# Performance work log

Hardware: AMD Instinct MI355X
Metric: run time of the kernel (lower is better)

Reference implementation:

```python
import jax, jax.numpy as jnp
import numpy as np

EMBED_DIM = 1024
NUM_HEADS = 16
DIM_K = EMBED_DIM // NUM_HEADS
B, S = 2, 2048


def setup_inputs() -> dict:
    key = jax.random.key(0)
    ks = jax.random.split(key, 7)
    scale = 1.0 / np.sqrt(EMBED_DIM)
    return {
        "query": jax.random.normal(ks[0], (B, S, EMBED_DIM), dtype=jnp.float32),
        "key": jax.random.normal(ks[1], (B, S, EMBED_DIM), dtype=jnp.float32),
        "value": jax.random.normal(ks[2], (B, S, EMBED_DIM), dtype=jnp.float32),
        "Wq": jax.random.normal(ks[3], (EMBED_DIM, EMBED_DIM), dtype=jnp.float32) * scale,
        "Wk": jax.random.normal(ks[4], (EMBED_DIM, EMBED_DIM), dtype=jnp.float32) * scale,
        "Wv": jax.random.normal(ks[5], (EMBED_DIM, EMBED_DIM), dtype=jnp.float32) * scale,
        "Wo": jax.random.normal(ks[6], (EMBED_DIM, EMBED_DIM), dtype=jnp.float32) * scale,
    }


def reference(query, key, value, Wq, Wk, Wv, Wo):
    b, s, e = query.shape
    # nn.Linear: y = x @ W.T  (bias=False)
    def proj(x, W):
        y = x @ W.T  # [b, s, e]
        return y.reshape(b, -1, NUM_HEADS, DIM_K).transpose(0, 2, 1, 3)  # [b, h, s, dk]

    q = proj(query, Wq)
    k = proj(key, Wk)
    v = proj(value, Wv)

    # attention: scores = q k^T / sqrt(dk); softmax; @ v  (dropout p=0 in eval)
    scores = jnp.einsum("bhqd,bhkd->bhqk", q, k) / jnp.sqrt(jnp.float32(DIM_K))
    attn = jax.nn.softmax(scores, axis=-1)
    x = jnp.einsum("bhqk,bhkd->bhqd", attn, v)  # [b, h, s, dk]

    x = x.transpose(0, 2, 1, 3).reshape(b, -1, e)  # merge heads
    return x @ Wo.T
```

## Files before the change

### kernel.cpp

```cpp
#include <hip/hip_runtime.h>
#include <hip/hip_bf16.h>
#include <stdint.h>

#define EMBED 1024
#define NHEAD 16
#define DKD   64
#define BATCH 2
#define SEQ   2048
#define MROWS (BATCH*SEQ)

typedef __attribute__((ext_vector_type(8)))  short bf16x8;
typedef __attribute__((ext_vector_type(4)))  float f32x4;
typedef __attribute__((ext_vector_type(16))) float f32x16;
typedef unsigned short u16;
typedef unsigned int   u32;
typedef __attribute__((ext_vector_type(4))) u32 u32x4;

__device__ inline u16 f2bf(float f) {
  return __builtin_bit_cast(u16, __float2bfloat16(f));
}

__device__ inline u32 cvtpk(float lo, float hi) {
  u32 r;
  asm("v_cvt_pk_bf16_f32 %0, %1, %2" : "=v"(r) : "v"(lo), "v"(hi));
  return r;
}

__device__ inline void plswap(u32& x, u32& y) {
  asm volatile("v_permlane32_swap_b32 %0, %1" : "+v"(x), "+v"(y));
}

__device__ inline void gload_lds16(const u16* g, u16* l) {
  __builtin_amdgcn_global_load_lds(
      (const __attribute__((address_space(1))) u32*)(const void*)g,
      (__attribute__((address_space(3))) u32*)(void*)l, 16, 0, 0);
}

__global__ __launch_bounds__(256) void cast_all(
    const float* __restrict__ s0, const float* __restrict__ s1,
    const float* __restrict__ s2, const float* __restrict__ s3,
    const float* __restrict__ s4, const float* __restrict__ s5,
    const float* __restrict__ s6,
    u16* __restrict__ d0, u16* __restrict__ d1, u16* __restrict__ d2,
    u16* __restrict__ d3, u16* __restrict__ d4, u16* __restrict__ d5,
    u16* __restrict__ d6) {
  const int y = blockIdx.y;
  const float* s; u16* d; int n4;
  switch (y) {
    case 0: s = s0; d = d0; n4 = MROWS*EMBED/4; break;
    case 1: s = s1; d = d1; n4 = MROWS*EMBED/4; break;
    case 2: s = s2; d = d2; n4 = MROWS*EMBED/4; break;
    case 3: s = s3; d = d3; n4 = EMBED*EMBED/4; break;
    case 4: s = s4; d = d4; n4 = EMBED*EMBED/4; break;
    case 5: s = s5; d = d5; n4 = EMBED*EMBED/4; break;
    default: s = s6; d = d6; n4 = EMBED*EMBED/4; break;
  }
  int i = blockIdx.x * 256 + threadIdx.x;
  int stride = gridDim.x * 256;
  for (int idx = i; idx < n4; idx += stride) {
    float4 f = ((const float4*)s)[idx];
    ushort4 o;
    o.x = f2bf(f.x); o.y = f2bf(f.y); o.z = f2bf(f.z); o.w = f2bf(f.w);
    ((ushort4*)d)[idx] = o;
  }
}

__global__ __launch_bounds__(256)
void gemm_qkv(const u16* __restrict__ A0, const u16* __restrict__ A1,
              const u16* __restrict__ A2, const u16* __restrict__ B0,
              const u16* __restrict__ B1, const u16* __restrict__ B2,
              u16* __restrict__ C0, u16* __restrict__ C1, u16* __restrict__ C2) {
  constexpr int K = EMBED;
  __shared__ u16 As[128 * 32];
  __shared__ u16 Bs[128 * 32];
  const int z = blockIdx.z;
  const u16* A = (z == 0) ? A0 : (z == 1) ? A1 : A2;
  const u16* B = (z == 0) ? B0 : (z == 1) ? B1 : B2;
  u16* C       = (z == 0) ? C0 : (z == 1) ? C1 : C2;

  const int t = threadIdx.x;
  const int w = t >> 6, l = t & 63;
  const int lr = l & 15, lg = l >> 4;
  const int m0 = blockIdx.x * 128;
  const int n0 = blockIdx.y * 128;
  const int wr = (w >> 1) * 64, wc = (w & 1) * 64;

  f32x4 acc[4][4] = {};

  const int srow = t >> 2;
  const int scol = (t & 3) * 8;
  const u16* Ag = A + (size_t)(m0 + srow) * K + scol;
  const u16* Bg = B + (size_t)(n0 + srow) * K + scol;
  u16* AsW = As + w * 512;
  u16* BsW = Bs + w * 512;
  const size_t rowstep = (size_t)64 * K;

  for (int k0 = 0; k0 < K; k0 += 32) {
    gload_lds16(Ag + k0,           AsW);
    gload_lds16(Ag + k0 + rowstep, AsW + 64 * 32);
    gload_lds16(Bg + k0,           BsW);
    gload_lds16(Bg + k0 + rowstep, BsW + 64 * 32);
    __syncthreads();
    bf16x8 a[4], b[4];
#pragma unroll
    for (int r = 0; r < 4; r++)
      a[r] = *(const bf16x8*)(As + (wr + r * 16 + lr) * 32 + 8 * lg);
#pragma unroll
    for (int c = 0; c < 4; c++)
      b[c] = *(const bf16x8*)(Bs + (wc + c * 16 + lr) * 32 + 8 * lg);
#pragma unroll
    for (int r = 0; r < 4; r++)
#pragma unroll
      for (int c = 0; c < 4; c++)
        acc[r][c] = __builtin_amdgcn_mfma_f32_16x16x32_bf16(a[r], b[c], acc[r][c], 0, 0, 0);
    __syncthreads();
  }

#pragma unroll
  for (int r = 0; r < 4; r++)
#pragma unroll
    for (int c = 0; c < 4; c++)
#pragma unroll
      for (int j = 0; j < 4; j++) {
        int m = m0 + wr + r * 16 + lg * 4 + j;
        int n = n0 + wc + c * 16 + lr;
        int b_ = m >> 11, s_ = m & 2047;
        int h_ = n >> 6,  d_ = n & 63;
        u16 vv = f2bf(acc[r][c][j]);
        if (z == 2)
          C[((size_t)(b_ * NHEAD + h_) * DKD + d_) * SEQ + s_] = vv;
        else
          C[(((size_t)(b_ * NHEAD + h_) * SEQ + s_) << 6) + d_] = vv;
      }
}

__global__ __launch_bounds__(256)
void gemm_out(const u16* __restrict__ A, const u16* __restrict__ B,
              float* __restrict__ C) {
  constexpr int K = EMBED, N = EMBED;
  __shared__ u16 As[64 * 32];
  __shared__ u16 Bs[128 * 32];
  const int t = threadIdx.x;
  const int w = t >> 6, l = t & 63;
  const int lr = l & 15, lg = l >> 4;
  const int m0 = blockIdx.x * 64;
  const int n0 = blockIdx.y * 128;
  const int wr = (w >> 1) * 32, wc = (w & 1) * 64;

  f32x4 acc[2][4] = {};

  const int srow = t >> 2;
  const int scol = (t & 3) * 8;
  const u16* Ag = A + (size_t)(m0 + srow) * K + scol;
  const u16* Bg = B + (size_t)(n0 + srow) * K + scol;
  u16* AsW = As + w * 512;
  u16* BsW = Bs + w * 512;
  const size_t rowstep = (size_t)64 * K;

  for (int k0 = 0; k0 < K; k0 += 32) {
    gload_lds16(Ag + k0,           AsW);
    gload_lds16(Bg + k0,           BsW);
    gload_lds16(Bg + k0 + rowstep, BsW + 64 * 32);
    __syncthreads();
    bf16x8 a[2], b[4];
#pragma unroll
    for (int r = 0; r < 2; r++)
      a[r] = *(const bf16x8*)(As + (wr + r * 16 + lr) * 32 + 8 * lg);
#pragma unroll
    for (int c = 0; c < 4; c++)
      b[c] = *(const bf16x8*)(Bs + (wc + c * 16 + lr) * 32 + 8 * lg);
#pragma unroll
    for (int r = 0; r < 2; r++)
#pragma unroll
      for (int c = 0; c < 4; c++)
        acc[r][c] = __builtin_amdgcn_mfma_f32_16x16x32_bf16(a[r], b[c], acc[r][c], 0, 0, 0);
    __syncthreads();
  }

#pragma unroll
  for (int r = 0; r < 2; r++)
#pragma unroll
    for (int c = 0; c < 4; c++)
#pragma unroll
      for (int j = 0; j < 4; j++) {
        int m = m0 + wr + r * 16 + lg * 4 + j;
        int n = n0 + wc + c * 16 + lr;
        C[(size_t)m * N + n] = acc[r][c][j];
      }
}

__global__ __launch_bounds__(256, 2)
void attn_kernel(const u16* __restrict__ Qh, const u16* __restrict__ Kh,
                 const u16* __restrict__ Vt, u16* __restrict__ Xo) {
  __shared__ u16 KV[4][8192];
  const int t = threadIdx.x, w = t >> 6, l = t & 63;
  const int q32 = l & 31, h = l >> 5;
  const int xcd = blockIdx.x & 7;
  const int li  = blockIdx.x >> 3;
  const int bh  = xcd * 4 + (li >> 4);
  const int qblk = li & 15;
  const int b_ = bh >> 4, h_ = bh & 15;
  const size_t base = (size_t)bh * SEQ * DKD;
  const u16* Kb = Kh + base;
  const u16* Vb = Vt + base;
  constexpr int NT = SEQ / 64;
  constexpr float C2 = 0.18033688f;
  constexpr float THR = 44.0f;

  const int qrow = qblk * 128 + w * 32 + q32;
  bf16x8 qf[4];
#pragma unroll
  for (int ks = 0; ks < 4; ks++)
    qf[ks] = *(const bf16x8*)(Qh + base + (size_t)qrow * DKD + ks * 16 + h * 8);

  f32x16 acc[2] = {};
  float m2 = -1e30f, lsum = 0.f;

  auto stage = [&](int slot, int kt) {
    u16* kd = &KV[slot][0];
    u16* vd = &KV[slot][4096];
    const int rb = w * 8 + (l >> 3);
    const int sg = (l & 7) ^ (l >> 3);
#pragma unroll
    for (int ch = 0; ch < 2; ch++) {
      int row = ch * 32 + rb;
      gload_lds16(Kb + (size_t)(kt * 64 + row) * DKD + sg * 8,
                  kd + (ch * 32 + w * 8) * 64);
      gload_lds16(Vb + (size_t)row * SEQ + kt * 64 + sg * 8,
                  vd + (ch * 32 + w * 8) * 64);
    }
  };

  auto qk = [&](const u16* kd, f32x16 (&s)[2]) {
#pragma unroll
    for (int c = 0; c < 2; c++) {
      int row = c * 32 + q32;
#pragma unroll
      for (int ks = 0; ks < 4; ks++) {
        bf16x8 kf = *(const bf16x8*)(kd + row * 64 + (((2 * ks + h) ^ (row & 7)) * 8));
        s[c] = __builtin_amdgcn_mfma_f32_32x32x16_bf16(kf, qf[ks], s[c], 0, 0, 0);
      }
    }
  };
  auto vload = [&](const u16* vd, bf16x8 (&vf)[2][4]) {
#pragma unroll
    for (int dc = 0; dc < 2; dc++) {
      int row = dc * 32 + q32;
#pragma unroll
      for (int tile = 0; tile < 4; tile++)
        vf[dc][tile] = *(const bf16x8*)(vd + row * 64 + (((2 * tile + h) ^ (row & 7)) * 8));
    }
  };
  auto softmax_pack = [&](f32x16 (&s)[2], bf16x8 (&pfrag)[4]) {
    float pm = s[0][0];
#pragma unroll
    for (int r = 1; r < 16; r++) pm = fmaxf(pm, s[0][r]);
#pragma unroll
    for (int r = 0; r < 16; r++) pm = fmaxf(pm, s[1][r]);
    if (__any(pm > m2 + THR)) {
      float pmo = __shfl_xor(pm, 32, 64);
      float mn = fmaxf(m2, fmaxf(pm, pmo));
      float al = __builtin_amdgcn_exp2f((m2 - mn) * C2);
      lsum *= al;
#pragma unroll
      for (int dc = 0; dc < 2; dc++)
#pragma unroll
        for (int r = 0; r < 16; r++) acc[dc][r] *= al;
      m2 = mn;
    }
    const float nm = -m2 * C2;
    float ls = 0.f;
#pragma unroll
    for (int c = 0; c < 2; c++) {
      float p[16];
#pragma unroll
      for (int r = 0; r < 16; r++) {
        p[r] = __builtin_amdgcn_exp2f(__builtin_fmaf(s[c][r], C2, nm));
        ls += p[r];
      }
      u32 Pk[8];
#pragma unroll
      for (int i = 0; i < 8; i++) Pk[i] = cvtpk(p[2 * i], p[2 * i + 1]);
      plswap(Pk[0], Pk[2]); plswap(Pk[1], Pk[3]);
      plswap(Pk[4], Pk[6]); plswap(Pk[5], Pk[7]);
      pfrag[2 * c]     = __builtin_bit_cast(bf16x8, (u32x4){Pk[0], Pk[1], Pk[2], Pk[3]});
      pfrag[2 * c + 1] = __builtin_bit_cast(bf16x8, (u32x4){Pk[4], Pk[5], Pk[6], Pk[7]});
    }
    lsum += ls;
  };
  auto pv = [&](bf16x8 (&vf)[2][4], bf16x8 (&pfrag)[4]) {
#pragma unroll
    for (int tile = 0; tile < 4; tile++)
#pragma unroll
      for (int dc = 0; dc < 2; dc++)
        acc[dc] = __builtin_amdgcn_mfma_f32_32x32x16_bf16(vf[dc][tile], pfrag[tile], acc[dc], 0, 0, 0);
  };

  stage(0, 0);
  stage(1, 1);
  __syncthreads();

  for (int kt = 0; kt < NT; kt += 2) {
    const int sA = kt & 3, sB = (kt + 1) & 3;
    if (kt + 2 < NT) {
      stage((kt + 2) & 3, kt + 2);
      stage((kt + 3) & 3, kt + 3);
    }
    f32x16 scA[2] = {}, scB[2] = {};
    qk(&KV[sA][0], scA);
    qk(&KV[sB][0], scB);
    bf16x8 vfA[2][4];
    vload(&KV[sA][4096], vfA);
    bf16x8 pfA[4];
    softmax_pack(scA, pfA);
    pv(vfA, pfA);
    bf16x8 vfB[2][4];
    vload(&KV[sB][4096], vfB);
    bf16x8 pfB[4];
    softmax_pack(scB, pfB);
    pv(vfB, pfB);
    __syncthreads();
  }

  lsum += __shfl_xor(lsum, 32, 64);
  float inv = 1.0f / lsum;
  u16* orow = Xo + ((size_t)b_ * SEQ + qrow) * EMBED + h_ * DKD;
#pragma unroll
  for (int dc = 0; dc < 2; dc++)
#pragma unroll
    for (int k4 = 0; k4 < 4; k4++) {
      u32 w0 = cvtpk(acc[dc][4 * k4 + 0] * inv, acc[dc][4 * k4 + 1] * inv);
      u32 w1 = cvtpk(acc[dc][4 * k4 + 2] * inv, acc[dc][4 * k4 + 3] * inv);
      int d = dc * 32 + k4 * 8 + h * 4;
      uint2 pk; pk.x = w0; pk.y = w1;
      *(uint2*)(orow + d) = pk;
    }
}

extern "C" void kernel_launch(void* const* d_in, const int* in_sizes, int n_in,
                              void* d_out, int out_size, void* d_ws, size_t ws_size,
                              hipStream_t stream) {
  const float* q  = (const float*)d_in[0];
  const float* k  = (const float*)d_in[1];
  const float* v  = (const float*)d_in[2];
  const float* Wq = (const float*)d_in[3];
  const float* Wk = (const float*)d_in[4];
  const float* Wv = (const float*)d_in[5];
  const float* Wo = (const float*)d_in[6];

  char* ws = (char*)d_ws;
  const size_t SZ_X = (size_t)MROWS * EMBED * 2;
  const size_t SZ_W = (size_t)EMBED * EMBED * 2;
  u16* qbf  = (u16*)(ws);
  u16* kbf  = (u16*)(ws + SZ_X);
  u16* vbf  = (u16*)(ws + 2 * SZ_X);
  u16* wqb  = (u16*)(ws + 3 * SZ_X);
  u16* wkb  = (u16*)(ws + 3 * SZ_X + SZ_W);
  u16* wvb  = (u16*)(ws + 3 * SZ_X + 2 * SZ_W);
  u16* wob  = (u16*)(ws + 3 * SZ_X + 3 * SZ_W);
  u16* Qh   = (u16*)(ws + 3 * SZ_X + 4 * SZ_W);
  u16* Kh   = (u16*)(ws + 4 * SZ_X + 4 * SZ_W);
  u16* Vt   = (u16*)(ws + 5 * SZ_X + 4 * SZ_W);
  u16* Xcat = (u16*)(ws + 6 * SZ_X + 4 * SZ_W);

  cast_all<<<dim3(1024, 7), 256, 0, stream>>>(q, k, v, Wq, Wk, Wv, Wo,
                                              qbf, kbf, vbf, wqb, wkb, wvb, wob);

  gemm_qkv<<<dim3(MROWS / 128, EMBED / 128, 3), 256, 0, stream>>>(
      qbf, kbf, vbf, wqb, wkb, wvb, Qh, Kh, Vt);

  attn_kernel<<<512, 256, 0, stream>>>(Qh, Kh, Vt, Xcat);

  gemm_out<<<dim3(MROWS / 64, EMBED / 128), 256, 0, stream>>>(Xcat, wob, (float*)d_out);
}
```

Measured before the change: 121.8 us.

## Fuse fp32-to-bf16 activation cast into QKV GEMM A-tile loading

Drops the separate cast of the query/key/value activations. The QKV GEMM now reads fp32 activations directly, converts them to bf16 in registers and stores them to LDS, with the next tile's loads software-prefetched ahead of the barrier. This removes a full write and re-read of three bf16 activation tensors plus most of the cast kernel's work. The price is that the GEMM reads fp32 A data redundantly across the 8 N-tile blocks and does register-staged LDS writes instead of direct global-to-LDS loads.

```diff
diff --git a/kernel.cpp b/kernel.cpp
--- a/kernel.cpp
+++ b/kernel.cpp
@@ -36,25 +36,15 @@
       (__attribute__((address_space(3))) u32*)(void*)l, 16, 0, 0);
 }
 
-__global__ __launch_bounds__(256) void cast_all(
+__global__ __launch_bounds__(256) void cast_w(
     const float* __restrict__ s0, const float* __restrict__ s1,
     const float* __restrict__ s2, const float* __restrict__ s3,
-    const float* __restrict__ s4, const float* __restrict__ s5,
-    const float* __restrict__ s6,
     u16* __restrict__ d0, u16* __restrict__ d1, u16* __restrict__ d2,
-    u16* __restrict__ d3, u16* __restrict__ d4, u16* __restrict__ d5,
-    u16* __restrict__ d6) {
+    u16* __restrict__ d3) {
   const int y = blockIdx.y;
-  const float* s; u16* d; int n4;
-  switch (y) {
-    case 0: s = s0; d = d0; n4 = MROWS*EMBED/4; break;
-    case 1: s = s1; d = d1; n4 = MROWS*EMBED/4; break;
-    case 2: s = s2; d = d2; n4 = MROWS*EMBED/4; break;
-    case 3: s = s3; d = d3; n4 = EMBED*EMBED/4; break;
-    case 4: s = s4; d = d4; n4 = EMBED*EMBED/4; break;
-    case 5: s = s5; d = d5; n4 = EMBED*EMBED/4; break;
-    default: s = s6; d = d6; n4 = EMBED*EMBED/4; break;
-  }
+  const float* s = (y == 0) ? s0 : (y == 1) ? s1 : (y == 2) ? s2 : s3;
+  u16* d        = (y == 0) ? d0 : (y == 1) ? d1 : (y == 2) ? d2 : d3;
+  constexpr int n4 = EMBED * EMBED / 4;
   int i = blockIdx.x * 256 + threadIdx.x;
   int stride = gridDim.x * 256;
   for (int idx = i; idx < n4; idx += stride) {
@@ -66,17 +56,17 @@
 }
 
 __global__ __launch_bounds__(256)
-void gemm_qkv(const u16* __restrict__ A0, const u16* __restrict__ A1,
-              const u16* __restrict__ A2, const u16* __restrict__ B0,
+void gemm_qkv(const float* __restrict__ A0, const float* __restrict__ A1,
+              const float* __restrict__ A2, const u16* __restrict__ B0,
               const u16* __restrict__ B1, const u16* __restrict__ B2,
               u16* __restrict__ C0, u16* __restrict__ C1, u16* __restrict__ C2) {
   constexpr int K = EMBED;
   __shared__ u16 As[128 * 32];
   __shared__ u16 Bs[128 * 32];
   const int z = blockIdx.z;
-  const u16* A = (z == 0) ? A0 : (z == 1) ? A1 : A2;
-  const u16* B = (z == 0) ? B0 : (z == 1) ? B1 : B2;
-  u16* C       = (z == 0) ? C0 : (z == 1) ? C1 : C2;
+  const float* A = (z == 0) ? A0 : (z == 1) ? A1 : A2;
+  const u16* B   = (z == 0) ? B0 : (z == 1) ? B1 : B2;
+  u16* C         = (z == 0) ? C0 : (z == 1) ? C1 : C2;
 
   const int t = threadIdx.x;
   const int w = t >> 6, l = t & 63;
@@ -89,17 +79,30 @@
 
   const int srow = t >> 2;
   const int scol = (t & 3) * 8;
-  const u16* Ag = A + (size_t)(m0 + srow) * K + scol;
-  const u16* Bg = B + (size_t)(n0 + srow) * K + scol;
-  u16* AsW = As + w * 512;
+  const float* Agf = A + (size_t)(m0 + srow) * K + scol;
+  const u16*   Bg  = B + (size_t)(n0 + srow) * K + scol;
   u16* BsW = Bs + w * 512;
   const size_t rowstep = (size_t)64 * K;
 
+  auto loadA = [&](float4 (&f)[4], int k0) {
+    f[0] = *(const float4*)(Agf + k0);
+    f[1] = *(const float4*)(Agf + k0 + 4);
+    f[2] = *(const float4*)(Agf + k0 + rowstep);
+    f[3] = *(const float4*)(Agf + k0 + rowstep + 4);
+  };
+
+  float4 fa[4];
+  loadA(fa, 0);
   for (int k0 = 0; k0 < K; k0 += 32) {
-    gload_lds16(Ag + k0,           AsW);
-    gload_lds16(Ag + k0 + rowstep, AsW + 64 * 32);
+    u32x4 pa0 = {cvtpk(fa[0].x, fa[0].y), cvtpk(fa[0].z, fa[0].w),
+                 cvtpk(fa[1].x, fa[1].y), cvtpk(fa[1].z, fa[1].w)};
+    u32x4 pa1 = {cvtpk(fa[2].x, fa[2].y), cvtpk(fa[2].z, fa[2].w),
+                 cvtpk(fa[3].x, fa[3].y), cvtpk(fa[3].z, fa[3].w)};
+    *(u32x4*)(As + w * 512 + l * 8)        = pa0;
+    *(u32x4*)(As + 2048 + w * 512 + l * 8) = pa1;
     gload_lds16(Bg + k0,           BsW);
     gload_lds16(Bg + k0 + rowstep, BsW + 64 * 32);
+    if (k0 + 32 < K) loadA(fa, k0 + 32);
     __syncthreads();
     bf16x8 a[4], b[4];
 #pragma unroll
@@ -351,9 +354,6 @@
   char* ws = (char*)d_ws;
   const size_t SZ_X = (size_t)MROWS * EMBED * 2;
   const size_t SZ_W = (size_t)EMBED * EMBED * 2;
-  u16* qbf  = (u16*)(ws);
-  u16* kbf  = (u16*)(ws + SZ_X);
-  u16* vbf  = (u16*)(ws + 2 * SZ_X);
   u16* wqb  = (u16*)(ws + 3 * SZ_X);
   u16* wkb  = (u16*)(ws + 3 * SZ_X + SZ_W);
   u16* wvb  = (u16*)(ws + 3 * SZ_X + 2 * SZ_W);
@@ -363,11 +363,10 @@
   u16* Vt   = (u16*)(ws + 5 * SZ_X + 4 * SZ_W);
   u16* Xcat = (u16*)(ws + 6 * SZ_X + 4 * SZ_W);
 
-  cast_all<<<dim3(1024, 7), 256, 0, stream>>>(q, k, v, Wq, Wk, Wv, Wo,
-                                              qbf, kbf, vbf, wqb, wkb, wvb, wob);
+  cast_w<<<dim3(128, 4), 256, 0, stream>>>(Wq, Wk, Wv, Wo, wqb, wkb, wvb, wob);
 
   gemm_qkv<<<dim3(MROWS / 128, EMBED / 128, 3), 256, 0, stream>>>(
-      qbf, kbf, vbf, wqb, wkb, wvb, Qh, Kh, Vt);
+      q, k, v, wqb, wkb, wvb, Qh, Kh, Vt);
 
   attn_kernel<<<512, 256, 0, stream>>>(Qh, Kh, Vt, Xcat);
 
```

Result: faster. 116.0 us (-4.7%).
